# Performance work log

Hardware: AMD Instinct MI355X
Metric: run time of the kernel (lower is better)

## Reference

```python
import jax, jax.numpy as jnp
import numpy as np
import math

NUM_CLASSES = 80
IOU_LOSS_THRESH = 0.5
ANCHORS = [
    np.array([[12, 16], [19, 36], [40, 28]], dtype=np.float32),
    np.array([[36, 75], [76, 55], [72, 146]], dtype=np.float32),
    np.array([[142, 110], [192, 243], [459, 401]], dtype=np.float32),
]


def decode(conv, anchors, stride, num_class):
    B, S = conv.shape[0], conv.shape[1]
    A = anchors.shape[0]
    conv = conv.reshape(B, S, S, A, 5 + num_class)
    dxdy = conv[..., 0:2]
    dwdh = conv[..., 2:4]
    dconf = conv[..., 4:5]
    dprob = conv[..., 5:]
    r = jnp.arange(S, dtype=conv.dtype)
    # matches torch: offset[..., 0] varies along dim2, offset[..., 1] along dim1
    offset = jnp.stack([jnp.broadcast_to(r[None, :], (S, S)),
                        jnp.broadcast_to(r[:, None], (S, S))], axis=-1)
    offset = offset[None, :, :, None, :]  # (1,S,S,1,2)
    pred_xy = (jax.nn.sigmoid(dxdy) + offset) * stride
    pred_wh = jnp.exp(dwdh) * jnp.asarray(anchors)  # (A,2) broadcast
    return jnp.concatenate([pred_xy, pred_wh,
                            jax.nn.sigmoid(dconf), jax.nn.sigmoid(dprob)], axis=-1)


def _to_corners(b):
    return jnp.concatenate([b[..., :2] - b[..., 2:] * 0.5,
                            b[..., :2] + b[..., 2:] * 0.5], axis=-1)


def bbox_ciou(boxes1, boxes2):
    b1 = _to_corners(boxes1)
    b2 = _to_corners(boxes2)
    b1 = jnp.concatenate([jnp.minimum(b1[..., :2], b1[..., 2:]),
                          jnp.maximum(b1[..., :2], b1[..., 2:])], axis=-1)
    b2 = jnp.concatenate([jnp.minimum(b2[..., :2], b2[..., 2:]),
                          jnp.maximum(b2[..., :2], b2[..., 2:])], axis=-1)
    area1 = (b1[..., 2] - b1[..., 0]) * (b1[..., 3] - b1[..., 1])
    area2 = (b2[..., 2] - b2[..., 0]) * (b2[..., 3] - b2[..., 1])
    lu = jnp.maximum(b1[..., :2], b2[..., :2])
    rd = jnp.minimum(b1[..., 2:], b2[..., 2:])
    inter = jnp.maximum(rd - lu, 0.0)
    inter_area = inter[..., 0] * inter[..., 1]
    union = area1 + area2 - inter_area
    iou = inter_area / (union + 1e-9)
    enc_lu = jnp.minimum(b1[..., :2], b2[..., :2])
    enc_rd = jnp.maximum(b1[..., 2:], b2[..., 2:])
    enc_wh = enc_rd - enc_lu
    c2 = enc_wh[..., 0] ** 2 + enc_wh[..., 1] ** 2
    p2 = (boxes1[..., 0] - boxes2[..., 0]) ** 2 + (boxes1[..., 1] - boxes2[..., 1]) ** 2
    atan1 = jnp.arctan(boxes1[..., 2] / (boxes1[..., 3] + 1e-9))
    atan2 = jnp.arctan(boxes2[..., 2] / (boxes2[..., 3] + 1e-9))
    v = 4.0 * (atan1 - atan2) ** 2 / (math.pi ** 2)
    a = v / (1.0 - iou + v)
    return iou - p2 / c2 - a * v


def bbox_iou(boxes1, boxes2):
    area1 = boxes1[..., 2] * boxes1[..., 3]
    area2 = boxes2[..., 2] * boxes2[..., 3]
    b1 = _to_corners(boxes1)
    b2 = _to_corners(boxes2)
    lu = jnp.maximum(b1[..., :2], b2[..., :2])
    rd = jnp.minimum(b1[..., 2:], b2[..., 2:])
    inter = jnp.maximum(rd - lu, 0.0)
    inter_area = inter[..., 0] * inter[..., 1]
    union = area1 + area2 - inter_area
    return inter_area / union


def loss_layer(conv, pred, label, bboxes, stride, num_class, iou_loss_thresh):
    B, S = conv.shape[0], conv.shape[1]
    input_size = float(stride * S)
    pred_xywh = pred[..., 0:4]
    pred_conf = pred[..., 4:5]
    pred_prob = pred[..., 5:]
    label_xywh = label[..., 0:4]
    respond_bbox = label[..., 4:5]
    label_prob = label[..., 5:]

    ciou = bbox_ciou(pred_xywh, label_xywh)[..., None]  # (B,S,S,3,1)
    bbox_loss_scale = 2.0 - label_xywh[..., 2:3] * label_xywh[..., 3:4] / input_size ** 2
    ciou_loss = respond_bbox * bbox_loss_scale * (1.0 - ciou)

    prob_pos = label_prob * (-jnp.log(pred_prob + 1e-9))
    prob_neg = (1.0 - label_prob) * (-jnp.log(1.0 - pred_prob + 1e-9))
    prob_loss = respond_bbox * (prob_pos + prob_neg)

    iou = bbox_iou(pred_xywh[:, :, :, :, None, :],
                   bboxes[:, None, None, None, :, :])  # (B,S,S,3,70)
    max_iou = jnp.max(iou, axis=-1, keepdims=True)
    respond_bgd = (1.0 - respond_bbox) * (max_iou < iou_loss_thresh).astype(pred.dtype)
    pos_loss = respond_bbox * (-jnp.log(pred_conf + 1e-9))
    neg_loss = respond_bgd * (-jnp.log(1.0 - pred_conf + 1e-9))
    conf_loss = pos_loss + neg_loss

    ciou_loss = ciou_loss.sum(axis=(1, 2, 3, 4)).mean()
    conf_loss = conf_loss.sum(axis=(1, 2, 3, 4)).mean()
    prob_loss = prob_loss.sum(axis=(1, 2, 3, 4)).mean()
    return ciou_loss, conf_loss, prob_loss


def setup_inputs() -> dict:
    key = jax.random.key(0)
    ks = jax.random.split(key, 7)
    B, NC = 16, NUM_CLASSES
    C = 3 * (5 + NC)
    inp = {
        'conv_lbbox': jax.random.normal(ks[0], (B, 19, 19, C), jnp.float32),
        'conv_mbbox': jax.random.normal(ks[1], (B, 38, 38, C), jnp.float32),
        'conv_sbbox': jax.random.normal(ks[2], (B, 76, 76, C), jnp.float32),
        'label_sbbox': jax.random.uniform(ks[3], (B, 76, 76, 3, 5 + NC), jnp.float32),
        'label_mbbox': jax.random.uniform(ks[4], (B, 38, 38, 3, 5 + NC), jnp.float32),
        'label_lbbox': jax.random.uniform(ks[5], (B, 19, 19, 3, 5 + NC), jnp.float32),
        'true_bboxes': jax.random.uniform(ks[6], (B, 70, 4), jnp.float32, 1.0, 600.0),
    }
    return inp


def reference(conv_lbbox, conv_mbbox, conv_sbbox, label_sbbox, label_mbbox,
              label_lbbox, true_bboxes):
    nc, thr = NUM_CLASSES, IOU_LOSS_THRESH
    pred_s = decode(conv_sbbox, ANCHORS[0], 8, nc)
    pred_m = decode(conv_mbbox, ANCHORS[1], 16, nc)
    pred_l = decode(conv_lbbox, ANCHORS[2], 32, nc)
    s_ciou, s_conf, s_prob = loss_layer(conv_sbbox, pred_s, label_sbbox, true_bboxes, 8, nc, thr)
    m_ciou, m_conf, m_prob = loss_layer(conv_mbbox, pred_m, label_mbbox, true_bboxes, 16, nc, thr)
    l_ciou, l_conf, l_prob = loss_layer(conv_lbbox, pred_l, label_lbbox, true_bboxes, 32, nc, thr)
    ciou_loss = s_ciou + m_ciou + l_ciou
    conf_loss = s_conf + m_conf + l_conf
    prob_loss = s_prob + m_prob + l_prob
    all_loss = ciou_loss + conf_loss + prob_loss
    return (all_loss, ciou_loss, conf_loss, prob_loss)
```

## Files before the change

### kernel.cpp

```cpp
#include <hip/hip_runtime.h>
#include <math.h>

#define NCLS 80
#define CH 85

static constexpr int RS = 16 * 76 * 76 * 3;
static constexpr int RM = 16 * 38 * 38 * 3;
static constexpr int RL = 16 * 19 * 19 * 3;

static constexpr int BS_BLK = RS / 256;
static constexpr int BM_BLK = (RM + 255) / 256;
static constexpr int BL_BLK = (RL + 255) / 256;
static constexpr int NBLK   = BS_BLK + BM_BLK + BL_BLK;

__constant__ float c_anchors[18] = {
    12.f, 16.f, 19.f, 36.f, 40.f, 28.f,
    36.f, 75.f, 76.f, 55.f, 72.f, 146.f,
    142.f, 110.f, 192.f, 243.f, 459.f, 401.f
};

__device__ __forceinline__ float fast_rcp(float x) {
    return __builtin_amdgcn_rcpf(x);
}
__device__ __forceinline__ float sigm(float x) {
    return fast_rcp(1.f + __expf(-x));
}
__device__ __forceinline__ float softplusf(float x) {
    return fmaxf(x, 0.f) + __logf(1.f + __expf(-fabsf(x)));
}

__global__ __launch_bounds__(256) void yolo_main(
    const float* __restrict__ conv_l, const float* __restrict__ conv_m,
    const float* __restrict__ conv_s, const float* __restrict__ lab_s,
    const float* __restrict__ lab_m, const float* __restrict__ lab_l,
    const float* __restrict__ tb, float* __restrict__ pb)
{
    int blk = blockIdx.x;

    const float* conv; const float* lab;
    int S; float stride; int ao; int blkLocal; int nrec_scale;
    if (blk < BS_BLK) {
        conv = conv_s; lab = lab_s; S = 76; stride = 8.f;  ao = 0;
        blkLocal = blk;                 nrec_scale = RS;
    } else if (blk < BS_BLK + BM_BLK) {
        conv = conv_m; lab = lab_m; S = 38; stride = 16.f; ao = 6;
        blkLocal = blk - BS_BLK;        nrec_scale = RM;
    } else {
        conv = conv_l; lab = lab_l; S = 19; stride = 32.f; ao = 12;
        blkLocal = blk - BS_BLK - BM_BLK; nrec_scale = RL;
    }

    int r0   = blkLocal * 256;
    int nrec = min(256, nrec_scale - r0);
    int E    = nrec * 85;
    int n4   = E >> 2;

    const float* cbase = conv + (size_t)r0 * CH;
    const float* lbase = lab  + (size_t)r0 * CH;

    __shared__ float convA[256 * 5];
    __shared__ float labA[256 * 5];

    float ciou_acc = 0.f, conf_acc = 0.f, prob_acc = 0.f;

    for (int i4 = threadIdx.x; i4 < n4; i4 += 256) {
        int e = i4 << 2;
        float4 cv = *reinterpret_cast<const float4*>(cbase + e);
        float4 lv = *reinterpret_cast<const float4*>(lbase + e);
        float cvv[4] = {cv.x, cv.y, cv.z, cv.w};
        float lvv[4] = {lv.x, lv.y, lv.z, lv.w};

        unsigned rA  = (unsigned)e / 85u;
        unsigned bnd = (rA + 1u) * 85u;
        float respA = lbase[rA * 85u + 4u];
        unsigned rB = ((unsigned)(e + 3) >= bnd) ? rA + 1u : rA;
        float respB = lbase[rB * 85u + 4u];

        #pragma unroll
        for (int d = 0; d < 4; d++) {
            unsigned el = (unsigned)(e + d);
            bool nxt   = el >= bnd;
            unsigned r = nxt ? rA + 1u : rA;
            unsigned c = el - r * 85u;
            float x = cvv[d], l = lvv[d];
            if (c >= 5u) {
                float sp = softplusf(x);
                float resp = nxt ? respB : respA;
                prob_acc += resp * (sp - l * x);
            } else {
                convA[r * 5u + c] = x;
                labA[r * 5u + c]  = l;
            }
        }
    }
    __syncthreads();

    int t = threadIdx.x;
    if (t < nrec) {
        unsigned rl = (unsigned)(r0 + t);
        unsigned a = rl % 3u; unsigned q = rl / 3u;
        unsigned j = q % (unsigned)S; q /= (unsigned)S;
        unsigned i = q % (unsigned)S; unsigned b = q / (unsigned)S;

        float c0 = convA[t * 5 + 0], c1 = convA[t * 5 + 1], c2v = convA[t * 5 + 2];
        float c3 = convA[t * 5 + 3], c4 = convA[t * 5 + 4];
        float lx = labA[t * 5 + 0], ly = labA[t * 5 + 1], lw = labA[t * 5 + 2];
        float lh = labA[t * 5 + 3], resp = labA[t * 5 + 4];

        float px = (sigm(c0) + (float)j) * stride;
        float py = (sigm(c1) + (float)i) * stride;
        float pw = __expf(c2v) * c_anchors[ao + 2 * a];
        float ph = __expf(c3)  * c_anchors[ao + 2 * a + 1];

        float hx = 0.5f * pw, hy = 0.5f * ph;
        float b1x1 = px - hx, b1y1 = py - hy, b1x2 = px + hx, b1y2 = py + hy;
        float hlx = 0.5f * lw, hly = 0.5f * lh;
        float b2x1 = lx - hlx, b2y1 = ly - hly, b2x2 = lx + hlx, b2y2 = ly + hly;

        float area1 = (b1x2 - b1x1) * (b1y2 - b1y1);
        float area2 = (b2x2 - b2x1) * (b2y2 - b2y1);
        float lux = fmaxf(b1x1, b2x1), luy = fmaxf(b1y1, b2y1);
        float rdx = fminf(b1x2, b2x2), rdy = fminf(b1y2, b2y2);
        float iw = fmaxf(rdx - lux, 0.f), ih = fmaxf(rdy - luy, 0.f);
        float inter = iw * ih;
        float uni = area1 + area2 - inter;
        float iou = inter / (uni + 1e-9f);

        float encw = fmaxf(b1x2, b2x2) - fminf(b1x1, b2x1);
        float ench = fmaxf(b1y2, b2y2) - fminf(b1y1, b2y1);
        float cc2 = encw * encw + ench * ench;
        float dx = px - lx, dy = py - ly;
        float p2 = dx * dx + dy * dy;
        float at1 = atanf(pw / (ph + 1e-9f));
        float at2 = atanf(lw / (lh + 1e-9f));
        float dat = at1 - at2;
        const float FOUR_OVER_PI2 = 0.40528473456935109f;
        float v = FOUR_OVER_PI2 * dat * dat;
        float al = v / (1.f - iou + v);
        float ciou = iou - p2 / cc2 - al * v;
        float bscale = 2.f - lw * lh * (1.f / (608.f * 608.f));
        ciou_acc = resp * bscale * (1.f - ciou);

        const float* tbp = tb + (size_t)b * 70 * 4;
        float parea = pw * ph;
        float maxiou = 0.f;
        for (int n = 0; n < 70; n++) {
            float tx = tbp[4 * n], ty = tbp[4 * n + 1];
            float tw = tbp[4 * n + 2], th = tbp[4 * n + 3];
            float tx1 = tx - 0.5f * tw, ty1 = ty - 0.5f * th;
            float tx2 = tx + 0.5f * tw, ty2 = ty + 0.5f * th;
            float ix1 = fmaxf(b1x1, tx1), iy1 = fmaxf(b1y1, ty1);
            float ix2 = fminf(b1x2, tx2), iy2 = fminf(b1y2, ty2);
            float iiw = fmaxf(ix2 - ix1, 0.f), iih = fmaxf(iy2 - iy1, 0.f);
            float ia = iiw * iih;
            float u = parea + tw * th - ia;
            maxiou = fmaxf(maxiou, ia * fast_rcp(u));
        }
        float rbgd = (1.f - resp) * (maxiou < 0.5f ? 1.f : 0.f);
        float spc = softplusf(c4);
        conf_acc = resp * (spc - c4) + rbgd * spc;
    }

    for (int off = 32; off > 0; off >>= 1) {
        ciou_acc += __shfl_down(ciou_acc, off);
        conf_acc += __shfl_down(conf_acc, off);
        prob_acc += __shfl_down(prob_acc, off);
    }
    __shared__ float red[4][3];
    int lane = threadIdx.x & 63, wv = threadIdx.x >> 6;
    if (lane == 0) { red[wv][0] = ciou_acc; red[wv][1] = conf_acc; red[wv][2] = prob_acc; }
    __syncthreads();
    if (threadIdx.x == 0) {
        pb[blk]            = red[0][0] + red[1][0] + red[2][0] + red[3][0];
        pb[NBLK + blk]     = red[0][1] + red[1][1] + red[2][1] + red[3][1];
        pb[2 * NBLK + blk] = red[0][2] + red[1][2] + red[2][2] + red[3][2];
    }
}

__global__ __launch_bounds__(256) void finalize_k(const float* __restrict__ pb,
                                                  float* __restrict__ out)
{
    double s0 = 0.0, s1 = 0.0, s2 = 0.0;
    for (int i = threadIdx.x; i < NBLK; i += 256) {
        s0 += (double)pb[i];
        s1 += (double)pb[NBLK + i];
        s2 += (double)pb[2 * NBLK + i];
    }
    for (int off = 32; off > 0; off >>= 1) {
        s0 += __shfl_down(s0, off);
        s1 += __shfl_down(s1, off);
        s2 += __shfl_down(s2, off);
    }
    __shared__ double rd[4][3];
    int lane = threadIdx.x & 63, wv = threadIdx.x >> 6;
    if (lane == 0) { rd[wv][0] = s0; rd[wv][1] = s1; rd[wv][2] = s2; }
    __syncthreads();
    if (threadIdx.x == 0) {
        float ci = (float)((rd[0][0] + rd[1][0] + rd[2][0] + rd[3][0]) / 16.0);
        float co = (float)((rd[0][1] + rd[1][1] + rd[2][1] + rd[3][1]) / 16.0);
        float pr = (float)((rd[0][2] + rd[1][2] + rd[2][2] + rd[3][2]) / 16.0);
        out[0] = ci + co + pr;
        out[1] = ci;
        out[2] = co;
        out[3] = pr;
    }
}

extern "C" void kernel_launch(void* const* d_in, const int* in_sizes, int n_in,
                              void* d_out, int out_size, void* d_ws, size_t ws_size,
                              hipStream_t stream) {
    const float* conv_l = (const float*)d_in[0];
    const float* conv_m = (const float*)d_in[1];
    const float* conv_s = (const float*)d_in[2];
    const float* lab_s  = (const float*)d_in[3];
    const float* lab_m  = (const float*)d_in[4];
    const float* lab_l  = (const float*)d_in[5];
    const float* tb     = (const float*)d_in[6];
    float* pb  = (float*)d_ws;
    float* out = (float*)d_out;

    yolo_main<<<NBLK, 256, 0, stream>>>(conv_l, conv_m, conv_s,
                                        lab_s, lab_m, lab_l, tb, pb);
    finalize_k<<<1, 256, 0, stream>>>(pb, out);
}
```

Before: 276.4 us.

## Halve records per block and drop branchy channel split in prob loss

Each block now covers 128 records instead of 256, so twice as many blocks run, and the first 5 channels are read directly per thread instead of being staged through shared memory. The prob loss is computed branch-free over all 85 channels, and the wrongly included first-5-channel terms are then subtracted per record. The record responsibility value is staged in shared memory, the full-block loop is unrolled, true boxes are read as float4, and launch bounds request higher occupancy. In exchange, half the threads sit idle during the IoU/max-IoU phase, and the subtraction step adds rounding differences and extra softplus work.

```diff
diff --git a/kernel.cpp b/kernel.cpp
--- a/kernel.cpp
+++ b/kernel.cpp
@@ -8,10 +8,15 @@
 static constexpr int RM = 16 * 38 * 38 * 3;
 static constexpr int RL = 16 * 19 * 19 * 3;
 
-static constexpr int BS_BLK = RS / 256;
-static constexpr int BM_BLK = (RM + 255) / 256;
-static constexpr int BL_BLK = (RL + 255) / 256;
+static constexpr int RECB = 128;
+static constexpr int BS_BLK = RS / RECB;
+static constexpr int BM_BLK = (RM + RECB - 1) / RECB;
+static constexpr int BL_BLK = (RL + RECB - 1) / RECB;
 static constexpr int NBLK   = BS_BLK + BM_BLK + BL_BLK;
+
+static constexpr int N4_FULL = RECB * CH / 4;
+static constexpr int K_FULL  = N4_FULL / 256;
+static constexpr int TAIL_T  = N4_FULL - K_FULL * 256;
 
 __constant__ float c_anchors[18] = {
     12.f, 16.f, 19.f, 36.f, 40.f, 28.f,
@@ -29,7 +34,7 @@
     return fmaxf(x, 0.f) + __logf(1.f + __expf(-fabsf(x)));
 }
 
-__global__ __launch_bounds__(256) void yolo_main(
+__global__ __launch_bounds__(256, 6) void yolo_main(
     const float* __restrict__ conv_l, const float* __restrict__ conv_m,
     const float* __restrict__ conv_s, const float* __restrict__ lab_s,
     const float* __restrict__ lab_m, const float* __restrict__ lab_l,
@@ -50,62 +55,73 @@
         blkLocal = blk - BS_BLK - BM_BLK; nrec_scale = RL;
     }
 
-    int r0   = blkLocal * 256;
-    int nrec = min(256, nrec_scale - r0);
-    int E    = nrec * 85;
-    int n4   = E >> 2;
+    int r0   = blkLocal * RECB;
+    int nrec = min(RECB, nrec_scale - r0);
+    int n4   = (nrec * CH) >> 2;
 
     const float* cbase = conv + (size_t)r0 * CH;
     const float* lbase = lab  + (size_t)r0 * CH;
 
-    __shared__ float convA[256 * 5];
-    __shared__ float labA[256 * 5];
-
-    float ciou_acc = 0.f, conf_acc = 0.f, prob_acc = 0.f;
-
-    for (int i4 = threadIdx.x; i4 < n4; i4 += 256) {
+    __shared__ float resp_s[RECB + 4];
+    __shared__ float red[4][3];
+
+    int t = threadIdx.x;
+
+    float resp = 0.f;
+    float c0 = 0.f, c1 = 0.f, c2v = 0.f, c3 = 0.f, c4 = 0.f;
+    float l0 = 0.f, l1 = 0.f, l2 = 0.f, l3 = 0.f;
+    if (t < nrec) {
+        const float* cr = cbase + (size_t)t * CH;
+        const float* lr = lbase + (size_t)t * CH;
+        resp = lr[4];
+        c0 = cr[0]; c1 = cr[1]; c2v = cr[2]; c3 = cr[3]; c4 = cr[4];
+        l0 = lr[0]; l1 = lr[1]; l2 = lr[2]; l3 = lr[3];
+    }
+    if (t <= RECB) resp_s[t] = (t < nrec) ? resp : 0.f;
+    __syncthreads();
+
+    float prob_acc = 0.f;
+
+    auto do4 = [&](int i4) {
         int e = i4 << 2;
         float4 cv = *reinterpret_cast<const float4*>(cbase + e);
         float4 lv = *reinterpret_cast<const float4*>(lbase + e);
-        float cvv[4] = {cv.x, cv.y, cv.z, cv.w};
-        float lvv[4] = {lv.x, lv.y, lv.z, lv.w};
-
         unsigned rA  = (unsigned)e / 85u;
-        unsigned bnd = (rA + 1u) * 85u;
-        float respA = lbase[rA * 85u + 4u];
-        unsigned rB = ((unsigned)(e + 3) >= bnd) ? rA + 1u : rA;
-        float respB = lbase[rB * 85u + 4u];
-
-        #pragma unroll
-        for (int d = 0; d < 4; d++) {
-            unsigned el = (unsigned)(e + d);
-            bool nxt   = el >= bnd;
-            unsigned r = nxt ? rA + 1u : rA;
-            unsigned c = el - r * 85u;
-            float x = cvv[d], l = lvv[d];
-            if (c >= 5u) {
-                float sp = softplusf(x);
-                float resp = nxt ? respB : respA;
-                prob_acc += resp * (sp - l * x);
-            } else {
-                convA[r * 5u + c] = x;
-                labA[r * 5u + c]  = l;
-            }
-        }
-    }
-    __syncthreads();
-
-    int t = threadIdx.x;
+        unsigned rem = (rA + 1u) * 85u - (unsigned)e;
+        float respA = resp_s[rA];
+        float respB = resp_s[rA + 1u];
+        float r1v = (rem <= 1u) ? respB : respA;
+        float r2v = (rem <= 2u) ? respB : respA;
+        float r3v = (rem <= 3u) ? respB : respA;
+        prob_acc = fmaf(respA, fmaf(-lv.x, cv.x, softplusf(cv.x)), prob_acc);
+        prob_acc = fmaf(r1v,   fmaf(-lv.y, cv.y, softplusf(cv.y)), prob_acc);
+        prob_acc = fmaf(r2v,   fmaf(-lv.z, cv.z, softplusf(cv.z)), prob_acc);
+        prob_acc = fmaf(r3v,   fmaf(-lv.w, cv.w, softplusf(cv.w)), prob_acc);
+    };
+
+    if (n4 == N4_FULL) {
+        #pragma unroll 5
+        for (int k = 0; k < K_FULL; ++k) do4(t + 256 * k);
+        if (t < TAIL_T) do4(t + 256 * K_FULL);
+    } else {
+        for (int i4 = t; i4 < n4; i4 += 256) do4(i4);
+    }
+
+    float ciou_acc = 0.f, conf_acc = 0.f;
     if (t < nrec) {
+        float corr = fmaf(-l0,   c0,  softplusf(c0))
+                   + fmaf(-l1,   c1,  softplusf(c1))
+                   + fmaf(-l2,   c2v, softplusf(c2v))
+                   + fmaf(-l3,   c3,  softplusf(c3))
+                   + fmaf(-resp, c4,  softplusf(c4));
+        prob_acc = fmaf(-resp, corr, prob_acc);
+
         unsigned rl = (unsigned)(r0 + t);
         unsigned a = rl % 3u; unsigned q = rl / 3u;
         unsigned j = q % (unsigned)S; q /= (unsigned)S;
         unsigned i = q % (unsigned)S; unsigned b = q / (unsigned)S;
 
-        float c0 = convA[t * 5 + 0], c1 = convA[t * 5 + 1], c2v = convA[t * 5 + 2];
-        float c3 = convA[t * 5 + 3], c4 = convA[t * 5 + 4];
-        float lx = labA[t * 5 + 0], ly = labA[t * 5 + 1], lw = labA[t * 5 + 2];
-        float lh = labA[t * 5 + 3], resp = labA[t * 5 + 4];
+        float lx = l0, ly = l1, lw = l2, lh = l3;
 
         float px = (sigm(c0) + (float)j) * stride;
         float py = (sigm(c1) + (float)i) * stride;
@@ -141,12 +157,13 @@
         float bscale = 2.f - lw * lh * (1.f / (608.f * 608.f));
         ciou_acc = resp * bscale * (1.f - ciou);
 
-        const float* tbp = tb + (size_t)b * 70 * 4;
+        const float4* tb4 = reinterpret_cast<const float4*>(tb) + (size_t)b * 70;
         float parea = pw * ph;
         float maxiou = 0.f;
+        #pragma unroll 5
         for (int n = 0; n < 70; n++) {
-            float tx = tbp[4 * n], ty = tbp[4 * n + 1];
-            float tw = tbp[4 * n + 2], th = tbp[4 * n + 3];
+            float4 tbx = tb4[n];
+            float tx = tbx.x, ty = tbx.y, tw = tbx.z, th = tbx.w;
             float tx1 = tx - 0.5f * tw, ty1 = ty - 0.5f * th;
             float tx2 = tx + 0.5f * tw, ty2 = ty + 0.5f * th;
             float ix1 = fmaxf(b1x1, tx1), iy1 = fmaxf(b1y1, ty1);
@@ -166,7 +183,6 @@
         conf_acc += __shfl_down(conf_acc, off);
         prob_acc += __shfl_down(prob_acc, off);
     }
-    __shared__ float red[4][3];
     int lane = threadIdx.x & 63, wv = threadIdx.x >> 6;
     if (lane == 0) { red[wv][0] = ciou_acc; red[wv][1] = conf_acc; red[wv][2] = prob_acc; }
     __syncthreads();
```

After: 273.8 us. About the same (-0.9%).
